# Performance work log

Measured on AMD Instinct MI355X. Metric: run time of the kernel, lower is better.

Reference implementation:

```python
import jax, jax.numpy as jnp
import numpy as np

ALPHA = 0.25
GAMMA = 2.0
W_CLASS = 2.0
W_BBOX = 5.0
W_GIOU = 2.0
EPS = 1e-8

B, N, C, M = 128, 900, 91, 100


def cxcywh_to_xyxy(b):
    cx, cy, w, h = jnp.split(b, 4, axis=-1)
    return jnp.concatenate([cx - 0.5 * w, cy - 0.5 * h, cx + 0.5 * w, cy + 0.5 * h], axis=-1)


def generalized_box_iou(a, b):
    # a: [B, N, 4], b: [B, M, 4], both xyxy -> giou [B, N, M]
    area_a = (a[..., 2] - a[..., 0]) * (a[..., 3] - a[..., 1])  # [B, N]
    area_b = (b[..., 2] - b[..., 0]) * (b[..., 3] - b[..., 1])  # [B, M]
    lt = jnp.maximum(a[:, :, None, :2], b[:, None, :, :2])      # [B, N, M, 2]
    rb = jnp.minimum(a[:, :, None, 2:], b[:, None, :, 2:])
    wh = jnp.clip(rb - lt, 0.0)
    inter = wh[..., 0] * wh[..., 1]                             # [B, N, M]
    union = area_a[:, :, None] + area_b[:, None, :] - inter
    iou = inter / union
    lt_e = jnp.minimum(a[:, :, None, :2], b[:, None, :, :2])
    rb_e = jnp.maximum(a[:, :, None, 2:], b[:, None, :, 2:])
    wh_e = jnp.clip(rb_e - lt_e, 0.0)
    area_e = wh_e[..., 0] * wh_e[..., 1]
    return iou - (area_e - union) / area_e


def setup_inputs() -> dict:
    key = jax.random.key(0)
    k1, k2, k3, k4 = jax.random.split(key, 4)
    pred_logits = jax.random.normal(k1, (B, N, C), dtype=jnp.float32)
    pred_boxes = jax.random.uniform(k2, (B, N, 4), dtype=jnp.float32)   # cxcywh in [0,1)
    tgt_labels = jax.random.randint(k3, (B, M), 0, C, dtype=jnp.int64 if jax.config.jax_enable_x64 else jnp.int32)
    tgt_boxes = jax.random.uniform(k4, (B, M, 4), dtype=jnp.float32)    # cxcywh in [0,1)
    return {"pred_logits": pred_logits, "pred_boxes": pred_boxes,
            "tgt_labels": tgt_labels, "tgt_boxes": tgt_boxes}


def reference(pred_logits, pred_boxes, tgt_labels, tgt_boxes):
    """Batched Hungarian-matcher cost matrix [B, N, M].

    Faithful to HungarianMatcher.forward's cost construction:
      cost = w_class * (pos_focal - neg_focal)[.., tgt_label]
           + w_bbox  * cdist_L1(pred_boxes, tgt_boxes)
           + w_giou  * (-GIoU(pred_xyxy, tgt_xyxy))
    The scipy linear_sum_assignment step is a host-side combinatorial solve
    on this matrix and is not part of the tensor math being baselined.
    """
    s = jax.nn.sigmoid(pred_logits)                              # [B, N, C]
    neg_cost = (1.0 - ALPHA) * s ** GAMMA * (-jnp.log(1.0 - s + EPS))
    pos_cost = ALPHA * (1.0 - s) ** GAMMA * (-jnp.log(s + EPS))
    cls_cost_full = pos_cost - neg_cost                          # [B, N, C]
    # gather per-target class costs -> [B, N, M]
    cost_class = jnp.take_along_axis(
        cls_cost_full, tgt_labels[:, None, :].astype(jnp.int32), axis=2)
    # L1 cdist over the 4 box coords -> [B, N, M]
    cost_bbox = jnp.sum(jnp.abs(pred_boxes[:, :, None, :] - tgt_boxes[:, None, :, :]), axis=-1)
    cost_giou = -generalized_box_iou(cxcywh_to_xyxy(pred_boxes), cxcywh_to_xyxy(tgt_boxes))
    return W_CLASS * cost_class + W_BBOX * cost_bbox + W_GIOU * cost_giou
```

## Files before the change

kernel.cpp:

```cpp
#include <hip/hip_runtime.h>

constexpr int B = 128, N = 900, C = 91, M = 100;
constexpr float ALPHA = 0.25f;
constexpr float W_CLASS = 2.0f;
constexpr float W_BBOX = 5.0f;
constexpr float W_GIOU = 2.0f;

constexpr int NBX  = 15;
constexpr int ROWS = N / NBX;
constexpr int BLK  = 256;
constexpr int MQ   = M / 4;
constexpr int NGRP = 10;
constexpr int KIT  = ROWS / NGRP;

__global__ __launch_bounds__(BLK) void hungarian_cost_kernel(
    const float* __restrict__ logits,
    const float* __restrict__ pboxes,
    const int*   __restrict__ tlabels,
    const float* __restrict__ tboxes,
    float* __restrict__ out)
{
    const int b   = blockIdx.y;
    const int n0  = blockIdx.x * ROWS;
    const int tid = threadIdx.x;

    const int mq   = tid % MQ;
    const int rgrp = tid / MQ;
    if (rgrp >= NGRP) return;

    const int r0 = rgrp * KIT;

    const float*  lb   = logits + ((size_t)b * N + n0 + r0) * C;
    const float4* pbt  = reinterpret_cast<const float4*>(pboxes) + (size_t)b * N + n0 + r0;
    float4*       outt = reinterpret_cast<float4*>(out) + ((size_t)(b * N + n0 + r0)) * MQ + mq;

    const int4 l4 = reinterpret_cast<const int4*>(tlabels + (size_t)b * M)[mq];
    const int labj[4] = {l4.x, l4.y, l4.z, l4.w};

    float4 pv[KIT];
    float  xsv[KIT][4];
    #pragma unroll
    for (int k = 0; k < KIT; ++k) {
        pv[k] = pbt[k];
        #pragma unroll
        for (int j = 0; j < 4; ++j) xsv[k][j] = lb[k * C + labj[j]];
    }

    float tx0[4], ty0[4], tx1[4], ty1[4], tar[4];
    {
        const float4* tbp = reinterpret_cast<const float4*>(tboxes) + (size_t)b * M;
        #pragma unroll
        for (int j = 0; j < 4; ++j) {
            const float4 t = tbp[mq * 4 + j];
            tx0[j] = t.x - 0.5f * t.z;  ty0[j] = t.y - 0.5f * t.w;
            tx1[j] = t.x + 0.5f * t.z;  ty1[j] = t.y + 0.5f * t.w;
            tar[j] = (tx1[j] - tx0[j]) * (ty1[j] - ty0[j]);
        }
    }

    #pragma unroll
    for (int k = 0; k < KIT; ++k) {
        const float4 p = pv[k];
        const float px0 = p.x - 0.5f * p.z, py0 = p.y - 0.5f * p.w;
        const float px1 = p.x + 0.5f * p.z, py1 = p.y + 0.5f * p.w;
        const float parea = (px1 - px0) * (py1 - py0);

        float4 res;
        float* rp = &res.x;
        #pragma unroll
        for (int j = 0; j < 4; ++j) {
            const float x    = xsv[k][j];
            const float e    = __expf(-x);
            const float onep = 1.0f + e;
            const float s    = __builtin_amdgcn_rcpf(onep);
            const float om   = e * s;
            const float L    = __logf(onep);
            const float ccls = W_CLASS * (ALPHA * om * om * L
                                        - (1.0f - ALPHA) * s * s * (x + L));

            const float dx0 = px0 - tx0[j], dx1 = px1 - tx1[j];
            const float dy0 = py0 - ty0[j], dy1 = py1 - ty1[j];
            const float l1 = 0.5f * (fabsf(dx0 + dx1) + fabsf(dy0 + dy1))
                           + fabsf(dx1 - dx0) + fabsf(dy1 - dy0);

            const float iw = fmaxf(fminf(px1, tx1[j]) - fmaxf(px0, tx0[j]), 0.0f);
            const float ih = fmaxf(fminf(py1, ty1[j]) - fmaxf(py0, ty0[j]), 0.0f);
            const float inter = iw * ih;
            const float uni   = parea + tar[j] - inter;

            const float ew = fmaxf(px1, tx1[j]) - fminf(px0, tx0[j]);
            const float eh = fmaxf(py1, ty1[j]) - fminf(py0, ty0[j]);
            const float earea = ew * eh;

            const float num  = inter * earea - uni * (earea - uni);
            const float rcpD = __builtin_amdgcn_rcpf(uni * earea);

            rp[j] = ccls + W_BBOX * l1 - W_GIOU * (num * rcpD);
        }

        outt[(size_t)k * MQ] = res;
    }
}

extern "C" void kernel_launch(void* const* d_in, const int* in_sizes, int n_in,
                              void* d_out, int out_size, void* d_ws, size_t ws_size,
                              hipStream_t stream) {
    const float* logits  = (const float*)d_in[0];
    const float* pboxes  = (const float*)d_in[1];
    const int*   tlabels = (const int*)d_in[2];
    const float* tboxes  = (const float*)d_in[3];
    float* out = (float*)d_out;

    dim3 grid(NBX, B);
    dim3 block(BLK);
    hipLaunchKernelGGL(hungarian_cost_kernel, grid, block, 0, stream,
                       logits, pboxes, tlabels, tboxes, out);
}
```

Before: 29.59 us.

## Precompute per-class focal cost into shared memory with coalesced logit loads

```diff
diff --git a/kernel.cpp b/kernel.cpp
--- a/kernel.cpp
+++ b/kernel.cpp
@@ -13,6 +13,10 @@
 constexpr int NGRP = 10;
 constexpr int KIT  = ROWS / NGRP;
 
+constexpr int NLOG  = ROWS * C;
+constexpr int NLOG4 = NLOG / 4;
+constexpr int SITER = (NLOG4 + BLK - 1) / BLK;
+
 __global__ __launch_bounds__(BLK) void hungarian_cost_kernel(
     const float* __restrict__ logits,
     const float* __restrict__ pboxes,
@@ -20,34 +24,28 @@
     const float* __restrict__ tboxes,
     float* __restrict__ out)
 {
+    __shared__ float cls[NLOG];
+
     const int b   = blockIdx.y;
     const int n0  = blockIdx.x * ROWS;
     const int tid = threadIdx.x;
 
-    const int mq   = tid % MQ;
-    const int rgrp = tid / MQ;
-    if (rgrp >= NGRP) return;
-
-    const int r0 = rgrp * KIT;
-
-    const float*  lb   = logits + ((size_t)b * N + n0 + r0) * C;
-    const float4* pbt  = reinterpret_cast<const float4*>(pboxes) + (size_t)b * N + n0 + r0;
-    float4*       outt = reinterpret_cast<float4*>(out) + ((size_t)(b * N + n0 + r0)) * MQ + mq;
-
-    const int4 l4 = reinterpret_cast<const int4*>(tlabels + (size_t)b * M)[mq];
-    const int labj[4] = {l4.x, l4.y, l4.z, l4.w};
+    const int  mq     = tid % MQ;
+    const int  rgrp   = tid / MQ;
+    const bool active = (rgrp < NGRP);
+    const int  r0     = rgrp * KIT;
 
     float4 pv[KIT];
-    float  xsv[KIT][4];
-    #pragma unroll
-    for (int k = 0; k < KIT; ++k) {
-        pv[k] = pbt[k];
+    float  tx0[4], ty0[4], tx1[4], ty1[4], tar[4];
+    int    labj[4];
+    if (active) {
+        const int4 l4 = reinterpret_cast<const int4*>(tlabels + (size_t)b * M)[mq];
+        labj[0] = l4.x; labj[1] = l4.y; labj[2] = l4.z; labj[3] = l4.w;
+
+        const float4* pbt = reinterpret_cast<const float4*>(pboxes) + (size_t)b * N + n0 + r0;
         #pragma unroll
-        for (int j = 0; j < 4; ++j) xsv[k][j] = lb[k * C + labj[j]];
-    }
+        for (int k = 0; k < KIT; ++k) pv[k] = pbt[k];
 
-    float tx0[4], ty0[4], tx1[4], ty1[4], tar[4];
-    {
         const float4* tbp = reinterpret_cast<const float4*>(tboxes) + (size_t)b * M;
         #pragma unroll
         for (int j = 0; j < 4; ++j) {
@@ -57,6 +55,46 @@
             tar[j] = (tx1[j] - tx0[j]) * (ty1[j] - ty0[j]);
         }
     }
+
+    const float4* lsrc4 = reinterpret_cast<const float4*>(
+        logits + ((size_t)b * N + n0) * C);
+    float4* clsv = reinterpret_cast<float4*>(cls);
+    #pragma unroll
+    for (int i = 0; i < SITER; ++i) {
+        const int idx = tid + i * BLK;
+        if (idx < NLOG4) {
+            const float4 v = lsrc4[idx];
+            float4 f;
+            const float* xp = &v.x;
+            float* fp = &f.x;
+            #pragma unroll
+            for (int u = 0; u < 4; ++u) {
+                const float x    = xp[u];
+                const float e    = __expf(-x);
+                const float onep = 1.0f + e;
+                const float s    = __builtin_amdgcn_rcpf(onep);
+                const float om   = e * s;
+                const float L    = __logf(onep);
+                fp[u] = W_CLASS * (ALPHA * om * om * L
+                                 - (1.0f - ALPHA) * s * s * (x + L));
+            }
+            clsv[idx] = f;
+        }
+    }
+    __syncthreads();
+
+    if (!active) return;
+
+    float xs[KIT][4];
+    #pragma unroll
+    for (int j = 0; j < 4; ++j) {
+        const float* cbase = cls + r0 * C + labj[j];
+        #pragma unroll
+        for (int k = 0; k < KIT; ++k) xs[k][j] = cbase[k * C];
+    }
+
+    float4* outt = reinterpret_cast<float4*>(out)
+                 + ((size_t)(b * N + n0 + r0)) * MQ + mq;
 
     #pragma unroll
     for (int k = 0; k < KIT; ++k) {
@@ -69,15 +107,6 @@
         float* rp = &res.x;
         #pragma unroll
         for (int j = 0; j < 4; ++j) {
-            const float x    = xsv[k][j];
-            const float e    = __expf(-x);
-            const float onep = 1.0f + e;
-            const float s    = __builtin_amdgcn_rcpf(onep);
-            const float om   = e * s;
-            const float L    = __logf(onep);
-            const float ccls = W_CLASS * (ALPHA * om * om * L
-                                        - (1.0f - ALPHA) * s * s * (x + L));
-
             const float dx0 = px0 - tx0[j], dx1 = px1 - tx1[j];
             const float dy0 = py0 - ty0[j], dy1 = py1 - ty1[j];
             const float l1 = 0.5f * (fabsf(dx0 + dx1) + fabsf(dy0 + dy1))
@@ -95,7 +124,7 @@
             const float num  = inter * earea - uni * (earea - uni);
             const float rcpD = __builtin_amdgcn_rcpf(uni * earea);
 
-            rp[j] = ccls + W_BBOX * l1 - W_GIOU * (num * rcpD);
+            rp[j] = xs[k][j] + W_BBOX * l1 - W_GIOU * (num * rcpD);
         }
 
         outt[(size_t)k * MQ] = res;
```

Measured after the change: 29.60 us. About the same (+0.0%).

## Stage logits tile and pred boxes into LDS via direct global-to-LDS loads

Applied to the files above, without the earlier changes.

```diff
diff --git a/kernel.cpp b/kernel.cpp
--- a/kernel.cpp
+++ b/kernel.cpp
@@ -13,6 +13,17 @@
 constexpr int NGRP = 10;
 constexpr int KIT  = ROWS / NGRP;
 
+constexpr int NLOG  = ROWS * C;
+constexpr int NLOG4 = NLOG / 4;
+constexpr int SIT   = (NLOG4 + BLK - 1) / BLK;
+
+__device__ __forceinline__ void gload_lds16(const void* g, void* l) {
+    __builtin_amdgcn_global_load_lds(
+        (const __attribute__((address_space(1))) void*)g,
+        (__attribute__((address_space(3))) void*)l,
+        16, 0, 0);
+}
+
 __global__ __launch_bounds__(BLK) void hungarian_cost_kernel(
     const float* __restrict__ logits,
     const float* __restrict__ pboxes,
@@ -20,34 +31,38 @@
     const float* __restrict__ tboxes,
     float* __restrict__ out)
 {
+    __shared__ float  slog[NLOG];
+    __shared__ float4 spb[ROWS];
+
     const int b   = blockIdx.y;
     const int n0  = blockIdx.x * ROWS;
     const int tid = threadIdx.x;
 
-    const int mq   = tid % MQ;
-    const int rgrp = tid / MQ;
-    if (rgrp >= NGRP) return;
+    const float4* lsrc4 = reinterpret_cast<const float4*>(
+        logits + ((size_t)b * N + n0) * C);
+    const float4* pbp = reinterpret_cast<const float4*>(pboxes) + (size_t)b * N + n0;
 
-    const int r0 = rgrp * KIT;
+    if (tid < ROWS)
+        gload_lds16(pbp + tid, spb);
 
-    const float*  lb   = logits + ((size_t)b * N + n0 + r0) * C;
-    const float4* pbt  = reinterpret_cast<const float4*>(pboxes) + (size_t)b * N + n0 + r0;
-    float4*       outt = reinterpret_cast<float4*>(out) + ((size_t)(b * N + n0 + r0)) * MQ + mq;
-
-    const int4 l4 = reinterpret_cast<const int4*>(tlabels + (size_t)b * M)[mq];
-    const int labj[4] = {l4.x, l4.y, l4.z, l4.w};
-
-    float4 pv[KIT];
-    float  xsv[KIT][4];
     #pragma unroll
-    for (int k = 0; k < KIT; ++k) {
-        pv[k] = pbt[k];
-        #pragma unroll
-        for (int j = 0; j < 4; ++j) xsv[k][j] = lb[k * C + labj[j]];
+    for (int i = 0; i < SIT; ++i) {
+        const int q = i * BLK + tid;
+        if (q < NLOG4) {
+            float4* ldst = reinterpret_cast<float4*>(slog) + (q & ~63);
+            gload_lds16(lsrc4 + q, ldst);
+        }
     }
 
+    const int  mq     = tid % MQ;
+    const int  rgrp   = tid / MQ;
+    const bool active = (rgrp < NGRP);
+
     float tx0[4], ty0[4], tx1[4], ty1[4], tar[4];
-    {
+    int   labj[4] = {0, 0, 0, 0};
+    if (active) {
+        const int4 l4 = reinterpret_cast<const int4*>(tlabels + (size_t)b * M)[mq];
+        labj[0] = l4.x; labj[1] = l4.y; labj[2] = l4.z; labj[3] = l4.w;
         const float4* tbp = reinterpret_cast<const float4*>(tboxes) + (size_t)b * M;
         #pragma unroll
         for (int j = 0; j < 4; ++j) {
@@ -58,9 +73,23 @@
         }
     }
 
-    #pragma unroll
+    __syncthreads();
+    if (!active) return;
+
+    const int r0 = rgrp * KIT;
+    float4* outt = reinterpret_cast<float4*>(out)
+                 + ((size_t)(b * N + n0 + r0)) * MQ + mq;
+
+    #pragma unroll 1
     for (int k = 0; k < KIT; ++k) {
-        const float4 p = pv[k];
+        const int row = r0 + k;
+        const float4 p = spb[row];
+
+        float xg[4];
+        #pragma unroll
+        for (int j = 0; j < 4; ++j)
+            xg[j] = slog[row * C + labj[j]];
+
         const float px0 = p.x - 0.5f * p.z, py0 = p.y - 0.5f * p.w;
         const float px1 = p.x + 0.5f * p.z, py1 = p.y + 0.5f * p.w;
         const float parea = (px1 - px0) * (py1 - py0);
@@ -69,7 +98,7 @@
         float* rp = &res.x;
         #pragma unroll
         for (int j = 0; j < 4; ++j) {
-            const float x    = xsv[k][j];
+            const float x    = xg[j];
             const float e    = __expf(-x);
             const float onep = 1.0f + e;
             const float s    = __builtin_amdgcn_rcpf(onep);
```

New measurement: 30.58 us. 3.3% more time.
